# Performance work log

Measured on AMD Instinct MI355X. Metric: run time of the kernel, lower is better.

Reference implementation:

```python
import jax, jax.numpy as jnp
import numpy as np

B, T, C = 2, 2048, 1024
H, D = 16, 64
EPS = 1e-05
SCALE = 1.0 / np.sqrt(D)


def _rmsnorm(x, w):
    # normalize over last dim (head_dim)
    return w * (x * jax.lax.rsqrt(jnp.mean(x * x, axis=-1, keepdims=True) + EPS))


def setup_inputs() -> dict:
    key = jax.random.key(0)
    ks = jax.random.split(key, 8)
    x = jax.random.normal(ks[0], (B, T, C), dtype=jnp.float32)
    # causal mask, 1 = attend, 0 = masked
    attention_mask = jnp.tril(jnp.ones((T, T), dtype=jnp.int32))[None, None]
    s = 1.0 / np.sqrt(C)
    Wq = jax.random.normal(ks[1], (C, H * D), dtype=jnp.float32) * s
    Wk = jax.random.normal(ks[2], (C, H * D), dtype=jnp.float32) * s
    Wv = jax.random.normal(ks[3], (C, H * D), dtype=jnp.float32) * s
    Wo = jax.random.normal(ks[4], (H * D, C), dtype=jnp.float32) * s
    q_norm_w = jnp.ones((D,), dtype=jnp.float32)
    k_norm_w = jnp.ones((D,), dtype=jnp.float32)
    gate = jnp.ones((1, H, 1, 1), dtype=jnp.float32)
    return {"x": x, "attention_mask": attention_mask, "Wq": Wq, "Wk": Wk,
            "Wv": Wv, "Wo": Wo, "q_norm_w": q_norm_w, "k_norm_w": k_norm_w,
            "gate": gate}


def reference(x, attention_mask, Wq, Wk, Wv, Wo, q_norm_w, k_norm_w, gate):
    Bx, Tx, Cx = x.shape
    vx = x @ Wv                                   # [B,T,H*D] (kept for value residual)
    q = (x @ Wq).reshape(Bx, Tx, H, D).transpose(0, 2, 1, 3)  # [B,H,T,D]
    k = (x @ Wk).reshape(Bx, Tx, H, D).transpose(0, 2, 1, 3)
    v = vx.reshape(Bx, Tx, H, D).transpose(0, 2, 1, 3)
    q = _rmsnorm(q, q_norm_w)
    k = _rmsnorm(k, k_norm_w)
    att = jnp.einsum('bhqd,bhkd->bhqk', q, k) * SCALE
    att = jnp.where(attention_mask == 0, -jnp.inf, att)
    att = jax.nn.softmax(att, axis=-1)
    att = att * gate                              # per-head gating after softmax
    out = jnp.einsum('bhqk,bhkd->bhqd', att, v)
    out = out.transpose(0, 2, 1, 3).reshape(Bx, Tx, Cx)
    out = out + vx                                # value residual
    out = out @ Wo
    return out
```

## Files before the change

kernel.cpp:

```cpp
#include <hip/hip_runtime.h>

#define T_SEQ 2048
#define CDIM 1024
#define NHEAD 16
#define HDIM 64
#define BATCH 2
#define EPSV 1e-5f
#define SCALE 0.125f
#define LOG2E 1.44269504088896f
#define SMAX 16.0f

typedef __attribute__((ext_vector_type(8))) short bf16x8;
typedef __attribute__((ext_vector_type(4))) float f32x4;

__device__ __forceinline__ float b2f(short s) {
  unsigned u = ((unsigned)(unsigned short)s) << 16;
  return __builtin_bit_cast(float, u);
}
__device__ __forceinline__ short f2b(float f) {
  unsigned u = __builtin_bit_cast(unsigned, f);
  unsigned r = (u + 0x7fffu + ((u >> 16) & 1u)) >> 16;
  return (short)r;
}
__device__ __forceinline__ unsigned cvt_pk_bf16(float a, float b) {
  unsigned r;
  asm("v_cvt_pk_bf16_f32 %0, %1, %2" : "=v"(r) : "v"(a), "v"(b));
  return r;
}

__device__ __forceinline__ void gld16(const void* g, void* l) {
  __builtin_amdgcn_global_load_lds((const __attribute__((address_space(1))) unsigned*)g,
                                   (__attribute__((address_space(3))) unsigned*)l, 16, 0, 0);
}

__device__ __forceinline__ void stage_sw(short* lds, const char* gbase, int gstride,
                                         int w, int l) {
#pragma unroll
  for (int i = 0; i < 2; ++i) {
    int chunk = w * 2048 + i * 1024 + l * 16;
    int row = chunk >> 7;
    int bir = chunk & 127;
    const char* src = gbase + (size_t)row * gstride + (bir ^ ((row & 7) << 4));
    gld16(src, (char*)lds + (w * 2048 + i * 1024));
  }
}

__global__ __launch_bounds__(256) void prep(const float* __restrict__ x,
                                            const float* __restrict__ Wq,
                                            const float* __restrict__ Wk,
                                            const float* __restrict__ Wv,
                                            const float* __restrict__ Wo,
                                            short* __restrict__ xb,
                                            short* __restrict__ WT) {
  __shared__ float tile[64][65];
  const int bid = blockIdx.x;
  if (bid < 2048) {
    size_t i = ((size_t)bid * 256 + threadIdx.x) * 8;
    float4 a = *(const float4*)&x[i];
    float4 b = *(const float4*)&x[i + 4];
    short4 lo, hi;
    lo.x = f2b(a.x); lo.y = f2b(a.y); lo.z = f2b(a.z); lo.w = f2b(a.w);
    hi.x = f2b(b.x); hi.y = f2b(b.y); hi.z = f2b(b.z); hi.w = f2b(b.w);
    *(short4*)&xb[i] = lo;
    *(short4*)&xb[i + 4] = hi;
    return;
  }
  const int t = bid - 2048;
  const int z = t >> 8, rem = t & 255;
  const float* W = (z == 0) ? Wq : (z == 1) ? Wk : (z == 2) ? Wv : Wo;
  const int r0 = (rem >> 4) * 64, c0 = (rem & 15) * 64;
  const int tr = threadIdx.x >> 4, tc4 = (threadIdx.x & 15) * 4;
#pragma unroll
  for (int i = 0; i < 4; ++i) {
    float4 v = *(const float4*)&W[(size_t)(r0 + tr + i * 16) * 1024 + c0 + tc4];
    tile[tr + i * 16][tc4 + 0] = v.x;
    tile[tr + i * 16][tc4 + 1] = v.y;
    tile[tr + i * 16][tc4 + 2] = v.z;
    tile[tr + i * 16][tc4 + 3] = v.w;
  }
  __syncthreads();
#pragma unroll
  for (int i = 0; i < 4; ++i) {
    int n = tr + i * 16;
    short4 o;
    o.x = f2b(tile[tc4 + 0][n]);
    o.y = f2b(tile[tc4 + 1][n]);
    o.z = f2b(tile[tc4 + 2][n]);
    o.w = f2b(tile[tc4 + 3][n]);
    *(short4*)&WT[((size_t)(z * 1024) + c0 + n) * 1024 + r0 + tc4] = o;
  }
}

template <int BN, bool F32OUT, bool NORM>
__global__ __launch_bounds__(256) void gemm_bf16(const short* __restrict__ A,
                                                 const short* __restrict__ Bt,
                                                 void* __restrict__ Cv,
                                                 const float* __restrict__ qw,
                                                 const float* __restrict__ kw,
                                                 int M, int N, int K, int nbx) {
  constexpr int NFR = BN / 32;
  constexpr int BITERS = BN / 64;
  __shared__ __attribute__((aligned(16))) short As[3][4096];
  __shared__ __attribute__((aligned(16))) short Bs[3][BN * 32];
  const int tid = threadIdx.x;
  const int w = tid >> 6, l = tid & 63;
  const int g = l >> 4, c = l & 15;
  const int wm = w >> 1, wn = w & 1;
  const int cpx = gridDim.x >> 3;
  const int wg = (blockIdx.x & 7) * cpx + (blockIdx.x >> 3);
  const int bx = wg % nbx, by = wg / nbx;
  const int m0 = by * 128, n0 = bx * BN;
  const char* Ab = (const char*)A;
  const char* Bb = (const char*)Bt;

  auto stage = [&](int k0, int buf) {
#pragma unroll
    for (int i = 0; i < 2; ++i) {
      int ci = w * 128 + i * 64 + l;
      int row = ci >> 2, c4 = ci & 3;
      gld16(Ab + ((size_t)(m0 + row) * K + k0) * 2 + ((c4 ^ (row & 3)) << 4),
            (char*)As[buf] + (w * 2048 + i * 1024));
    }
#pragma unroll
    for (int i = 0; i < BITERS; ++i) {
      int ci = w * (64 * BITERS) + i * 64 + l;
      int row = ci >> 2, c4 = ci & 3;
      gld16(Bb + ((size_t)(n0 + row) * K + k0) * 2 + ((c4 ^ (row & 3)) << 4),
            (char*)Bs[buf] + (w * (1024 * BITERS) + i * 1024));
    }
  };

  f32x4 acc[4][NFR];
#pragma unroll
  for (int mt = 0; mt < 4; ++mt)
#pragma unroll
    for (int nt = 0; nt < NFR; ++nt) {
      f32x4 z = {0.f, 0.f, 0.f, 0.f};
      acc[mt][nt] = z;
    }

  const int NT = K >> 5;
  stage(0, 0);
  stage(32, 1);
  if constexpr (BITERS == 2) asm volatile("s_waitcnt vmcnt(4)" ::: "memory");
  else                       asm volatile("s_waitcnt vmcnt(3)" ::: "memory");
  __builtin_amdgcn_s_barrier();
  __builtin_amdgcn_sched_barrier(0);

  int cbuf = 0;
  for (int t = 0; t < NT; ++t) {
    int tgt = cbuf + 2; if (tgt >= 3) tgt -= 3;
    if (t + 2 < NT) stage((t + 2) << 5, tgt);
    bf16x8 a[4], bf[NFR];
#pragma unroll
    for (int mt = 0; mt < 4; ++mt) {
      const int row = wm * 64 + mt * 16 + c;
      a[mt] = *(const bf16x8*)&As[cbuf][row * 32 + ((g ^ (row & 3)) << 3)];
    }
#pragma unroll
    for (int nt = 0; nt < NFR; ++nt) {
      const int row = wn * (BN / 2) + nt * 16 + c;
      bf[nt] = *(const bf16x8*)&Bs[cbuf][row * 32 + ((g ^ (row & 3)) << 3)];
    }
    __builtin_amdgcn_s_setprio(1);
#pragma unroll
    for (int mt = 0; mt < 4; ++mt)
#pragma unroll
      for (int nt = 0; nt < NFR; ++nt)
        acc[mt][nt] = __builtin_amdgcn_mfma_f32_16x16x32_bf16(a[mt], bf[nt], acc[mt][nt], 0, 0, 0);
    __builtin_amdgcn_s_setprio(0);
    if (t + 1 < NT) {
      if (t + 2 < NT) {
        if constexpr (BITERS == 2) asm volatile("s_waitcnt vmcnt(4)" ::: "memory");
        else                       asm volatile("s_waitcnt vmcnt(3)" ::: "memory");
      } else {
        asm volatile("s_waitcnt vmcnt(0)" ::: "memory");
      }
      __builtin_amdgcn_s_barrier();
      __builtin_amdgcn_sched_barrier(0);
    }
    cbuf = cbuf + 1; if (cbuf >= 3) cbuf -= 3;
  }

  if constexpr (NORM) {
    if (n0 < 2048) {
      const float* wgt = (n0 < 1024) ? qw : kw;
      const float scl = (n0 < 1024) ? SCALE * LOG2E : 1.f;
      float w4[NFR];
#pragma unroll
      for (int nt = 0; nt < NFR; ++nt) w4[nt] = wgt[nt * 16 + c] * scl;
#pragma unroll
      for (int mt = 0; mt < 4; ++mt)
#pragma unroll
        for (int r = 0; r < 4; ++r) {
          float s = 0.f;
#pragma unroll
          for (int nt = 0; nt < NFR; ++nt) s += acc[mt][nt][r] * acc[mt][nt][r];
          s += __shfl_xor(s, 1);
          s += __shfl_xor(s, 2);
          s += __shfl_xor(s, 4);
          s += __shfl_xor(s, 8);
          const float rstd = rsqrtf(s * (1.0f / 64.0f) + EPSV);
#pragma unroll
          for (int nt = 0; nt < NFR; ++nt) acc[mt][nt][r] *= rstd * w4[nt];
        }
    }
  }

  if constexpr (F32OUT) {
    float* C = (float*)Cv;
#pragma unroll
    for (int mt = 0; mt < 4; ++mt)
#pragma unroll
      for (int nt = 0; nt < NFR; ++nt)
#pragma unroll
        for (int r = 0; r < 4; ++r)
          C[(size_t)(m0 + wm * 64 + mt * 16 + 4 * g + r) * N + n0 + wn * (BN / 2) + nt * 16 + c] =
              acc[mt][nt][r];
  } else {
    short* C = (short*)Cv;
#pragma unroll
    for (int mt = 0; mt < 4; ++mt)
#pragma unroll
      for (int nt = 0; nt < NFR; ++nt)
#pragma unroll
        for (int r = 0; r < 4; ++r)
          C[(size_t)(m0 + wm * 64 + mt * 16 + 4 * g + r) * N + n0 + wn * (BN / 2) + nt * 16 + c] =
              f2b(acc[mt][nt][r]);
  }
}

__global__ __launch_bounds__(256) void vt_kernel(const short* __restrict__ QKV,
                                                 short* __restrict__ VT) {
  __shared__ short tile[64][66];
  const int t0 = blockIdx.x * 64;
  const int h = blockIdx.y, b = blockIdx.z;
  const int tid = threadIdx.x;
  const int r = tid >> 3, c8 = (tid & 7) * 8;
#pragma unroll
  for (int p = 0; p < 2; ++p) {
    int row = r + p * 32;
    bf16x8 v = *(const bf16x8*)&QKV[(size_t)(b * T_SEQ + t0 + row) * 3072 + 2048 + h * 64 + c8];
#pragma unroll
    for (int j = 0; j < 8; ++j) tile[row][c8 + j] = v[j];
  }
  __syncthreads();
#pragma unroll
  for (int p = 0; p < 2; ++p) {
    int d = r + p * 32;
    short o[8];
#pragma unroll
    for (int j = 0; j < 8; ++j) o[j] = tile[c8 + j][d];
    *(bf16x8*)&VT[((size_t)(b * NHEAD + h) * 64 + d) * T_SEQ + t0 + c8] = *(bf16x8*)o;
  }
}

__global__ __launch_bounds__(256) void attn_fwd(const short* __restrict__ QKV,
                                                const short* __restrict__ VT,
                                                const float* __restrict__ gate,
                                                short* __restrict__ Ob) {
  __shared__ __attribute__((aligned(16))) short pool[20480];
  short* Qs = pool;
  short* Ksb = pool + 4096;
  short* Vsb = pool + 12288;

  const int bid = blockIdx.x;
  const int xcd = bid & 7, s = bid >> 3;
  const int a = s & 31, bq = s >> 5, k4 = a >> 2;
  const int qt = (bq == 0) ? 31 - k4 : (bq == 1) ? k4 : (bq == 2) ? 23 - k4 : 8 + k4;
  const int bh = xcd * 4 + (a & 3);
  const int h = bh & 15, b = bh >> 4;
  const int q0 = qt * 64;
  const int tid = threadIdx.x;
  const int w = tid >> 6, l = tid & 63;
  const int g = l >> 4, c = l & 15;

  const char* qkb = (const char*)QKV;
  const char* kbase = qkb + ((size_t)(b * T_SEQ) * 3072 + 1024 + h * 64) * 2;
  const char* vtb = (const char*)VT + ((size_t)(b * NHEAD + h) * 64) * T_SEQ * 2;
  const float gh = gate[h];

  stage_sw(Qs, qkb + ((size_t)(b * T_SEQ + q0) * 3072 + h * 64) * 2, 3072 * 2, w, l);
  stage_sw(Ksb, kbase, 3072 * 2, w, l);
  stage_sw(Vsb, vtb, T_SEQ * 2, w, l);
  __syncthreads();

  bf16x8 qf[2];
  {
    const int row = w * 16 + c;
#pragma unroll
    for (int ks = 0; ks < 2; ++ks)
      qf[ks] = *(const bf16x8*)&Qs[row * 64 + ((ks * 32 + g * 8) ^ ((row & 7) << 3))];
  }
  short* ps = pool + (w << 10);

  f32x4 oacc[4];
#pragma unroll
  for (int dt = 0; dt < 4; ++dt) {
    f32x4 z = {0.f, 0.f, 0.f, 0.f};
    oacc[dt] = z;
  }
  float lpart = 0.f;
  int cur = 0;

  for (int kt = 0; kt <= qt; ++kt) {
    if (kt < qt) {
      stage_sw(Ksb + ((cur ^ 1) << 12), kbase + (size_t)(kt + 1) * 64 * 3072 * 2, 3072 * 2, w, l);
      stage_sw(Vsb + ((cur ^ 1) << 12), vtb + (size_t)(kt + 1) * 64 * 2, T_SEQ * 2, w, l);
    }
    f32x4 sacc[4];
#pragma unroll
    for (int mt = 0; mt < 4; ++mt) {
      f32x4 z = {-SMAX, -SMAX, -SMAX, -SMAX};
      sacc[mt] = z;
    }
    __builtin_amdgcn_s_setprio(1);
#pragma unroll
    for (int mt = 0; mt < 4; ++mt) {
      const int row = mt * 16 + c;
#pragma unroll
      for (int ks = 0; ks < 2; ++ks) {
        bf16x8 kf = *(const bf16x8*)&Ksb[(cur << 12) + row * 64 + ((ks * 32 + g * 8) ^ ((row & 7) << 3))];
        sacc[mt] = __builtin_amdgcn_mfma_f32_16x16x32_bf16(kf, qf[ks], sacc[mt], 0, 0, 0);
      }
    }
    __builtin_amdgcn_s_setprio(0);
    bf16x8 vf[4][2];
#pragma unroll
    for (int dt = 0; dt < 4; ++dt) {
      const int row = dt * 16 + c;
#pragma unroll
      for (int ks = 0; ks < 2; ++ks)
        vf[dt][ks] = *(const bf16x8*)&Vsb[(cur << 12) + row * 64 + ((ks * 32 + g * 8) ^ ((row & 7) << 3))];
    }
    if (kt == qt) {
#pragma unroll
      for (int mt = 0; mt < 4; ++mt)
#pragma unroll
        for (int r = 0; r < 4; ++r)
          if (mt * 16 + 4 * g + r > w * 16 + c) sacc[mt][r] = -1e30f;
    }
#pragma unroll
    for (int mt = 0; mt < 4; ++mt) {
      float p0 = exp2f(sacc[mt][0]);
      float p1 = exp2f(sacc[mt][1]);
      float p2 = exp2f(sacc[mt][2]);
      float p3 = exp2f(sacc[mt][3]);
      lpart += (p0 + p1) + (p2 + p3);
      uint2 pk;
      pk.x = cvt_pk_bf16(p0, p1);
      pk.y = cvt_pk_bf16(p2, p3);
      *(uint2*)&ps[(c << 6) + ((mt * 16 + 4 * g) ^ ((c & 7) << 3))] = pk;
    }
    bf16x8 pb[2];
#pragma unroll
    for (int ks = 0; ks < 2; ++ks)
      pb[ks] = *(const bf16x8*)&ps[(c << 6) + ((ks * 32 + g * 8) ^ ((c & 7) << 3))];
    __builtin_amdgcn_s_setprio(1);
#pragma unroll
    for (int dt = 0; dt < 4; ++dt)
#pragma unroll
      for (int ks = 0; ks < 2; ++ks)
        oacc[dt] = __builtin_amdgcn_mfma_f32_16x16x32_bf16(vf[dt][ks], pb[ks], oacc[dt], 0, 0, 0);
    __builtin_amdgcn_s_setprio(0);
    __syncthreads();
    cur ^= 1;
  }
  float lsum = lpart;
  lsum += __shfl_xor(lsum, 16);
  lsum += __shfl_xor(lsum, 32);
  const float gl = gh / lsum;
  const short* Vr = QKV + (size_t)(b * T_SEQ + q0 + w * 16 + c) * 3072 + 2048 + h * 64;
  short* Oro = Ob + (size_t)(b * T_SEQ + q0 + w * 16 + c) * 1024 + h * 64;
#pragma unroll
  for (int dt = 0; dt < 4; ++dt) {
    const int d0 = dt * 16 + 4 * g;
    short4 vres = *(const short4*)&Vr[d0];
    short4 o;
    o.x = f2b(oacc[dt][0] * gl + b2f(vres.x));
    o.y = f2b(oacc[dt][1] * gl + b2f(vres.y));
    o.z = f2b(oacc[dt][2] * gl + b2f(vres.z));
    o.w = f2b(oacc[dt][3] * gl + b2f(vres.w));
    *(short4*)&Oro[d0] = o;
  }
}

extern "C" void kernel_launch(void* const* d_in, const int* in_sizes, int n_in,
                              void* d_out, int out_size, void* d_ws, size_t ws_size,
                              hipStream_t stream) {
  const float* x  = (const float*)d_in[0];
  const float* Wq = (const float*)d_in[2];
  const float* Wk = (const float*)d_in[3];
  const float* Wv = (const float*)d_in[4];
  const float* Wo = (const float*)d_in[5];
  const float* qw = (const float*)d_in[6];
  const float* kw = (const float*)d_in[7];
  const float* gate = (const float*)d_in[8];
  float* out = (float*)d_out;

  char* ws = (char*)d_ws;
  short* xb  = (short*)ws;
  short* WT  = (short*)(ws + ((size_t)8 << 20));
  short* QKV = (short*)(ws + ((size_t)16 << 20));
  short* VTb = (short*)(ws + ((size_t)40 << 20));
  short* Obf = (short*)(ws + ((size_t)48 << 20));

  const int M = BATCH * T_SEQ;

  prep<<<3072, 256, 0, stream>>>(x, Wq, Wk, Wv, Wo, xb, WT);
  gemm_bf16<128, false, true><<<768, 256, 0, stream>>>(xb, WT, QKV, qw, kw, M, 3072, CDIM, 24);
  vt_kernel<<<dim3(32, 16, 2), 256, 0, stream>>>(QKV, VTb);
  attn_fwd<<<1024, 256, 0, stream>>>(QKV, VTb, gate, Obf);
  gemm_bf16<64, true, false><<<512, 256, 0, stream>>>(Obf, WT + (size_t)3072 * 1024, out,
                                                      nullptr, nullptr, M, CDIM, CDIM, 16);
}
```

Before: 114.6 us.

## Use 128-row query tiles with 8 waves sharing K/V stages in attention

The attention kernel now processes 128 query rows per block with 512 threads, so each staged 64-key K/V tile feeds eight waves instead of four, halving K/V global-to-LDS traffic per query. Waves whose rows are fully masked for a key tile skip its compute, and the causal mask uses a per-wave offset. The softmax row sum moves from scalar adds plus cross-lane shuffles to an extra MFMA of P against a ones vector. The trade-off is fewer, larger blocks with more LDS per block and some idle waves on the diagonal tiles.

Result: no change. 114.6 us (-0.0%).

```diff
diff --git a/kernel.cpp b/kernel.cpp
--- a/kernel.cpp
+++ b/kernel.cpp
@@ -41,8 +41,16 @@
     int row = chunk >> 7;
     int bir = chunk & 127;
     const char* src = gbase + (size_t)row * gstride + (bir ^ ((row & 7) << 4));
-    gld16(src, (char*)lds + (w * 2048 + i * 1024));
-  }
+    gld16(src, (char*)lds + chunk);
+  }
+}
+__device__ __forceinline__ void stage_sw8(short* lds, const char* gbase, int gstride,
+                                          int w, int l) {
+  int chunk = w * 1024 + l * 16;
+  int row = chunk >> 7;
+  int bir = chunk & 127;
+  const char* src = gbase + (size_t)row * gstride + (bir ^ ((row & 7) << 4));
+  gld16(src, (char*)lds + chunk);
 }
 
 __global__ __launch_bounds__(256) void prep(const float* __restrict__ x,
@@ -255,22 +263,20 @@
   }
 }
 
-__global__ __launch_bounds__(256) void attn_fwd(const short* __restrict__ QKV,
-                                                const short* __restrict__ VT,
-                                                const float* __restrict__ gate,
-                                                short* __restrict__ Ob) {
-  __shared__ __attribute__((aligned(16))) short pool[20480];
-  short* Qs = pool;
-  short* Ksb = pool + 4096;
-  short* Vsb = pool + 12288;
+__global__ __launch_bounds__(512, 4) void attn_fwd(const short* __restrict__ QKV,
+                                                   const short* __restrict__ VT,
+                                                   const float* __restrict__ gate,
+                                                   short* __restrict__ Ob) {
+  __shared__ __attribute__((aligned(16))) short pool[24576];
 
   const int bid = blockIdx.x;
   const int xcd = bid & 7, s = bid >> 3;
-  const int a = s & 31, bq = s >> 5, k4 = a >> 2;
-  const int qt = (bq == 0) ? 31 - k4 : (bq == 1) ? k4 : (bq == 2) ? 23 - k4 : 8 + k4;
-  const int bh = xcd * 4 + (a & 3);
+  const int t8 = (s >> 2) & 7;
+  const int Q16 = (s < 32) ? 15 - t8 : t8;
+  const int bh = xcd * 4 + (s & 3);
   const int h = bh & 15, b = bh >> 4;
-  const int q0 = qt * 64;
+  const int q0 = Q16 * 128;
+  const int nkt = 2 * Q16 + 2;
   const int tid = threadIdx.x;
   const int w = tid >> 6, l = tid & 63;
   const int g = l >> 4, c = l & 15;
@@ -280,9 +286,9 @@
   const char* vtb = (const char*)VT + ((size_t)(b * NHEAD + h) * 64) * T_SEQ * 2;
   const float gh = gate[h];
 
-  stage_sw(Qs, qkb + ((size_t)(b * T_SEQ + q0) * 3072 + h * 64) * 2, 3072 * 2, w, l);
-  stage_sw(Ksb, kbase, 3072 * 2, w, l);
-  stage_sw(Vsb, vtb, T_SEQ * 2, w, l);
+  stage_sw(pool, qkb + ((size_t)(b * T_SEQ + q0) * 3072 + h * 64) * 2, 3072 * 2, w, l);
+  stage_sw8(pool + 8192, kbase, 3072 * 2, w, l);
+  stage_sw8(pool + 16384, vtb, T_SEQ * 2, w, l);
   __syncthreads();
 
   bf16x8 qf[2];
@@ -290,9 +296,13 @@
     const int row = w * 16 + c;
 #pragma unroll
     for (int ks = 0; ks < 2; ++ks)
-      qf[ks] = *(const bf16x8*)&Qs[row * 64 + ((ks * 32 + g * 8) ^ ((row & 7) << 3))];
+      qf[ks] = *(const bf16x8*)&pool[row * 64 + ((ks * 32 + g * 8) ^ ((row & 7) << 3))];
   }
   short* ps = pool + (w << 10);
+
+  bf16x8 onesf;
+#pragma unroll
+  for (int j = 0; j < 8; ++j) onesf[j] = (short)0x3F80;
 
   f32x4 oacc[4];
 #pragma unroll
@@ -300,78 +310,82 @@
     f32x4 z = {0.f, 0.f, 0.f, 0.f};
     oacc[dt] = z;
   }
-  float lpart = 0.f;
+  f32x4 oacc4 = {0.f, 0.f, 0.f, 0.f};
   int cur = 0;
 
-  for (int kt = 0; kt <= qt; ++kt) {
-    if (kt < qt) {
-      stage_sw(Ksb + ((cur ^ 1) << 12), kbase + (size_t)(kt + 1) * 64 * 3072 * 2, 3072 * 2, w, l);
-      stage_sw(Vsb + ((cur ^ 1) << 12), vtb + (size_t)(kt + 1) * 64 * 2, T_SEQ * 2, w, l);
-    }
-    f32x4 sacc[4];
-#pragma unroll
-    for (int mt = 0; mt < 4; ++mt) {
-      f32x4 z = {-SMAX, -SMAX, -SMAX, -SMAX};
-      sacc[mt] = z;
-    }
-    __builtin_amdgcn_s_setprio(1);
-#pragma unroll
-    for (int mt = 0; mt < 4; ++mt) {
-      const int row = mt * 16 + c;
-#pragma unroll
-      for (int ks = 0; ks < 2; ++ks) {
-        bf16x8 kf = *(const bf16x8*)&Ksb[(cur << 12) + row * 64 + ((ks * 32 + g * 8) ^ ((row & 7) << 3))];
-        sacc[mt] = __builtin_amdgcn_mfma_f32_16x16x32_bf16(kf, qf[ks], sacc[mt], 0, 0, 0);
-      }
-    }
-    __builtin_amdgcn_s_setprio(0);
-    bf16x8 vf[4][2];
-#pragma unroll
-    for (int dt = 0; dt < 4; ++dt) {
-      const int row = dt * 16 + c;
+  for (int kt = 0; kt < nkt; ++kt) {
+    if (kt + 1 < nkt) {
+      stage_sw8(pool + 8192 + ((cur ^ 1) << 12), kbase + (size_t)(kt + 1) * 64 * 3072 * 2, 3072 * 2, w, l);
+      stage_sw8(pool + 16384 + ((cur ^ 1) << 12), vtb + (size_t)(kt + 1) * 64 * 2, T_SEQ * 2, w, l);
+    }
+    const short* Ks = pool + 8192 + (cur << 12);
+    const short* Vs = pool + 16384 + (cur << 12);
+    const int dq = q0 + w * 16 - kt * 64;
+    if (dq > -16) {
+      f32x4 sacc[4];
+#pragma unroll
+      for (int mt = 0; mt < 4; ++mt) {
+        f32x4 z = {-SMAX, -SMAX, -SMAX, -SMAX};
+        sacc[mt] = z;
+      }
+      __builtin_amdgcn_s_setprio(1);
+#pragma unroll
+      for (int mt = 0; mt < 4; ++mt) {
+        const int row = mt * 16 + c;
+#pragma unroll
+        for (int ks = 0; ks < 2; ++ks) {
+          bf16x8 kf = *(const bf16x8*)&Ks[row * 64 + ((ks * 32 + g * 8) ^ ((row & 7) << 3))];
+          sacc[mt] = __builtin_amdgcn_mfma_f32_16x16x32_bf16(kf, qf[ks], sacc[mt], 0, 0, 0);
+        }
+      }
+      __builtin_amdgcn_s_setprio(0);
+      bf16x8 vf[4][2];
+#pragma unroll
+      for (int dt = 0; dt < 4; ++dt) {
+        const int row = dt * 16 + c;
+#pragma unroll
+        for (int ks = 0; ks < 2; ++ks)
+          vf[dt][ks] = *(const bf16x8*)&Vs[row * 64 + ((ks * 32 + g * 8) ^ ((row & 7) << 3))];
+      }
+      if (dq < 63) {
+#pragma unroll
+        for (int mt = 0; mt < 4; ++mt)
+#pragma unroll
+          for (int r = 0; r < 4; ++r)
+            if (mt * 16 + 4 * g + r > dq + c) sacc[mt][r] = -1e30f;
+      }
+#pragma unroll
+      for (int mt = 0; mt < 4; ++mt) {
+        float p0 = exp2f(sacc[mt][0]);
+        float p1 = exp2f(sacc[mt][1]);
+        float p2 = exp2f(sacc[mt][2]);
+        float p3 = exp2f(sacc[mt][3]);
+        uint2 pk;
+        pk.x = cvt_pk_bf16(p0, p1);
+        pk.y = cvt_pk_bf16(p2, p3);
+        *(uint2*)&ps[(c << 6) + ((mt * 16 + 4 * g) ^ ((c & 7) << 3))] = pk;
+      }
+      bf16x8 pb[2];
 #pragma unroll
       for (int ks = 0; ks < 2; ++ks)
-        vf[dt][ks] = *(const bf16x8*)&Vsb[(cur << 12) + row * 64 + ((ks * 32 + g * 8) ^ ((row & 7) << 3))];
-    }
-    if (kt == qt) {
-#pragma unroll
-      for (int mt = 0; mt < 4; ++mt)
-#pragma unroll
-        for (int r = 0; r < 4; ++r)
-          if (mt * 16 + 4 * g + r > w * 16 + c) sacc[mt][r] = -1e30f;
-    }
-#pragma unroll
-    for (int mt = 0; mt < 4; ++mt) {
-      float p0 = exp2f(sacc[mt][0]);
-      float p1 = exp2f(sacc[mt][1]);
-      float p2 = exp2f(sacc[mt][2]);
-      float p3 = exp2f(sacc[mt][3]);
-      lpart += (p0 + p1) + (p2 + p3);
-      uint2 pk;
-      pk.x = cvt_pk_bf16(p0, p1);
-      pk.y = cvt_pk_bf16(p2, p3);
-      *(uint2*)&ps[(c << 6) + ((mt * 16 + 4 * g) ^ ((c & 7) << 3))] = pk;
-    }
-    bf16x8 pb[2];
-#pragma unroll
-    for (int ks = 0; ks < 2; ++ks)
-      pb[ks] = *(const bf16x8*)&ps[(c << 6) + ((ks * 32 + g * 8) ^ ((c & 7) << 3))];
-    __builtin_amdgcn_s_setprio(1);
-#pragma unroll
-    for (int dt = 0; dt < 4; ++dt)
-#pragma unroll
-      for (int ks = 0; ks < 2; ++ks)
-        oacc[dt] = __builtin_amdgcn_mfma_f32_16x16x32_bf16(vf[dt][ks], pb[ks], oacc[dt], 0, 0, 0);
-    __builtin_amdgcn_s_setprio(0);
+        pb[ks] = *(const bf16x8*)&ps[(c << 6) + ((ks * 32 + g * 8) ^ ((c & 7) << 3))];
+      __builtin_amdgcn_s_setprio(1);
+#pragma unroll
+      for (int dt = 0; dt < 4; ++dt)
+#pragma unroll
+        for (int ks = 0; ks < 2; ++ks)
+          oacc[dt] = __builtin_amdgcn_mfma_f32_16x16x32_bf16(vf[dt][ks], pb[ks], oacc[dt], 0, 0, 0);
+      oacc4 = __builtin_amdgcn_mfma_f32_16x16x32_bf16(onesf, pb[0], oacc4, 0, 0, 0);
+      oacc4 = __builtin_amdgcn_mfma_f32_16x16x32_bf16(onesf, pb[1], oacc4, 0, 0, 0);
+      __builtin_amdgcn_s_setprio(0);
+    }
     __syncthreads();
     cur ^= 1;
   }
-  float lsum = lpart;
-  lsum += __shfl_xor(lsum, 16);
-  lsum += __shfl_xor(lsum, 32);
-  const float gl = gh / lsum;
-  const short* Vr = QKV + (size_t)(b * T_SEQ + q0 + w * 16 + c) * 3072 + 2048 + h * 64;
-  short* Oro = Ob + (size_t)(b * T_SEQ + q0 + w * 16 + c) * 1024 + h * 64;
+  const float gl = gh / oacc4[0];
+  const int qrow = q0 + w * 16 + c;
+  const short* Vr = QKV + (size_t)(b * T_SEQ + qrow) * 3072 + 2048 + h * 64;
+  short* Oro = Ob + (size_t)(b * T_SEQ + qrow) * 1024 + h * 64;
 #pragma unroll
   for (int dt = 0; dt < 4; ++dt) {
     const int d0 = dt * 16 + 4 * g;
@@ -410,7 +424,7 @@
   prep<<<3072, 256, 0, stream>>>(x, Wq, Wk, Wv, Wo, xb, WT);
   gemm_bf16<128, false, true><<<768, 256, 0, stream>>>(xb, WT, QKV, qw, kw, M, 3072, CDIM, 24);
   vt_kernel<<<dim3(32, 16, 2), 256, 0, stream>>>(QKV, VTb);
-  attn_fwd<<<1024, 256, 0, stream>>>(QKV, VTb, gate, Obf);
+  attn_fwd<<<512, 512, 0, stream>>>(QKV, VTb, gate, Obf);
   gemm_bf16<64, true, false><<<512, 256, 0, stream>>>(Obf, WT + (size_t)3072 * 1024, out,
                                                       nullptr, nullptr, M, CDIM, CDIM, 16);
 }
```
